# Kernel tuning notes

Hardware: AMD Instinct MI355X
Metric: run time of the kernel (lower is better)

Reference implementation:

```python
import jax, jax.numpy as jnp
import numpy as np

N = 4096      # num_nodes
F = 256       # node_dim
K = 4         # num_heads
FP = 64       # out_dim per head
P_EDGE = 0.008  # edge probability (~33 avg degree)


def setup_inputs() -> dict:
    key = jax.random.key(0)
    k1, k2, k3, k4, k5 = jax.random.split(key, 5)
    x = jax.random.normal(k1, (N, F), dtype=jnp.float32)
    # binary adjacency mask with self loops so every row has a neighbor
    adj = (jax.random.uniform(k2, (N, N)) < P_EDGE).astype(jnp.float32)
    mask = jnp.maximum(adj, jnp.eye(N, dtype=jnp.float32))
    batch = jnp.zeros((N,), dtype=jnp.int32)  # unused (is_final_layer=False)
    # xavier-style init for W (node_dim -> K*FP) and attention vectors
    w_scale = np.sqrt(2.0 / (F + K * FP)).astype(np.float32)
    W = jax.random.normal(k3, (F, K * FP), dtype=jnp.float32) * w_scale
    b = jnp.zeros((K * FP,), dtype=jnp.float32)
    a_scale = np.sqrt(2.0 / (K * FP + 1)).astype(np.float32)
    a_left = jax.random.normal(k4, (1, K, FP), dtype=jnp.float32) * a_scale
    a_right = jax.random.normal(k5, (1, K, FP), dtype=jnp.float32) * a_scale
    return {"x": x, "mask": mask, "batch": batch, "W": W, "b": b,
            "a_left": a_left, "a_right": a_right}


def reference(x, mask, batch, W, b, a_left, a_right):
    # dropout prob = 0.0 (eval mode) -> identity
    x_proj = (x @ W + b).reshape(N, K, FP)                 # (N,K,F')
    score_src = (x_proj * a_left).sum(axis=-1)             # (N,K)
    score_tgt = (x_proj * a_right).sum(axis=-1)            # (N,K)
    score = score_src[:, None, :] + score_tgt[None, :, :]  # (N,N,K)
    score = jax.nn.leaky_relu(score, negative_slope=0.2)
    # non-standard global mean/std normalization (torch .std() is unbiased)
    score = (score - score.mean()) / score.std(ddof=1)
    score = jnp.exp(score)
    m = mask[:, :, None]                                   # (N,N,1)
    denom = (score * m).sum(axis=1, keepdims=True)         # (N,1,K)
    aij = (score / denom) * m                              # (N,N,K)
    attention = jnp.transpose(aij, (2, 0, 1))              # (K,N,N)
    h_prime = jnp.einsum('knm,mkf->nkf', attention, x_proj)  # (N,K,F')
    h_prime = jax.nn.elu(h_prime)
    # is_final_layer=False -> concat heads
    return h_prime.reshape(N, K * FP)
```

## Files before the change

### kernel.cpp

```cpp
#include <hip/hip_runtime.h>
#include <hip/hip_bf16.h>
#include <math.h>

#define NN 4096
#define FF 256
#define KH 4
#define FP 64
#define NCOL 256
#define MAXNBR 512
#define SCAN_BLKS 4096
#define GEMM_BLKS 512
#define MOM_BLOCKS 1024
#define MOM_ROWS 4

__device__ __forceinline__ float bits2f(unsigned b) {
    union { unsigned u; float f; } c; c.u = b << 16; return c.f;
}
__device__ __forceinline__ int is_fp32(const void* mask) {
    return ((const unsigned*)mask)[0] == 0x3F800000u;
}

#define OFF_PART   0
#define OFF_MUSIG  65536
#define OFF_XP     131072
#define OFF_SRC    4325376
#define OFF_TGT    4390912
#define OFF_NBR    4456448
#define OFF_CNT    8650752

__global__ __launch_bounds__(256) void k_scores(
        const void* __restrict__ xr, const void* __restrict__ mask,
        const void* __restrict__ Wr, const void* __restrict__ br,
        const void* __restrict__ alr, const void* __restrict__ arr,
        float* __restrict__ srcb, float* __restrict__ tgtb) {
    const int fl = is_fp32(mask);
    const int tid = threadIdx.x;
    __shared__ float al_s[NCOL], ar_s[NCOL];
    __shared__ float wl_s[FF][KH], wr_s[FF][KH];
    __shared__ float bl_s[KH], brr_s[KH];

    if (fl) {
        al_s[tid] = ((const float*)alr)[tid];
        ar_s[tid] = ((const float*)arr)[tid];
    } else {
        al_s[tid] = bits2f(((const unsigned short*)alr)[tid]);
        ar_s[tid] = bits2f(((const unsigned short*)arr)[tid]);
    }
    __syncthreads();

    if (tid < 8) {
        int k = tid & 3, which = tid >> 2;
        float s = 0.f;
        for (int f = 0; f < FP; ++f) {
            int cc = k * FP + f;
            float bvv = fl ? ((const float*)br)[cc]
                           : bits2f(((const unsigned short*)br)[cc]);
            s += bvv * (which ? ar_s[cc] : al_s[cc]);
        }
        if (which) brr_s[k] = s; else bl_s[k] = s;
    }

    {
        const float* WrowF = (const float*)Wr + (size_t)tid * NCOL;
        const unsigned short* WrowB = (const unsigned short*)Wr + (size_t)tid * NCOL;
        #pragma unroll
        for (int k = 0; k < KH; ++k) {
            float sl = 0.f, sr = 0.f;
            for (int f = 0; f < FP; ++f) {
                int cc = k * FP + f;
                float w = fl ? WrowF[cc] : bits2f(WrowB[cc]);
                sl += w * al_s[cc];
                sr += w * ar_s[cc];
            }
            wl_s[tid][k] = sl;
            wr_s[tid][k] = sr;
        }
    }
    __syncthreads();

    const int r = tid & 63, k = tid >> 6;
    const int n = blockIdx.x * 64 + r;
    float sl = bl_s[k], sr = brr_s[k];
    if (fl) {
        const float4* xrow = (const float4*)((const float*)xr + (size_t)n * FF);
        for (int j4 = 0; j4 < FF / 4; ++j4) {
            float4 xv = xrow[j4];
            int j = j4 * 4;
            sl += xv.x * wl_s[j][k] + xv.y * wl_s[j+1][k] + xv.z * wl_s[j+2][k] + xv.w * wl_s[j+3][k];
            sr += xv.x * wr_s[j][k] + xv.y * wr_s[j+1][k] + xv.z * wr_s[j+2][k] + xv.w * wr_s[j+3][k];
        }
    } else {
        const ushort4* xrow = (const ushort4*)((const unsigned short*)xr + (size_t)n * FF);
        for (int j4 = 0; j4 < FF / 4; ++j4) {
            ushort4 u = xrow[j4];
            float x0 = bits2f(u.x), x1 = bits2f(u.y), x2 = bits2f(u.z), x3 = bits2f(u.w);
            int j = j4 * 4;
            sl += x0 * wl_s[j][k] + x1 * wl_s[j+1][k] + x2 * wl_s[j+2][k] + x3 * wl_s[j+3][k];
            sr += x0 * wr_s[j][k] + x1 * wr_s[j+1][k] + x2 * wr_s[j+2][k] + x3 * wr_s[j+3][k];
        }
    }
    srcb[n * KH + k] = sl;
    tgtb[n * KH + k] = sr;
}

__global__ __launch_bounds__(256) void k_fused(
        const void* __restrict__ xr, const void* __restrict__ mask,
        const void* __restrict__ Wr, const void* __restrict__ br,
        float* __restrict__ xp,
        const float* __restrict__ srcb, const float* __restrict__ tgtb,
        unsigned short* __restrict__ nbr_g, int* __restrict__ cnt_g,
        double2* __restrict__ partials) {
    const int fl = is_fp32(mask);
    const int tid = threadIdx.x;
    __shared__ union {
        float4 xs[8][64];
        struct { unsigned short snbr[MAXNBR]; int cnt; } sc;
        struct { double l1[256], l2[256]; } mo;
    } sm;

    if (blockIdx.x < GEMM_BLKS) {
        int n0 = blockIdx.x * 8;
        if (fl) {
            const float4* xq = (const float4*)xr;
            for (int t = tid; t < 512; t += 256) {
                int r = t >> 6, q = t & 63;
                sm.xs[r][q] = xq[(size_t)(n0 + r) * 64 + q];
            }
        } else {
            const ushort4* xq = (const ushort4*)xr;
            for (int t = tid; t < 512; t += 256) {
                int r = t >> 6, q = t & 63;
                ushort4 u = xq[(size_t)(n0 + r) * 64 + q];
                float4 v; v.x = bits2f(u.x); v.y = bits2f(u.y); v.z = bits2f(u.z); v.w = bits2f(u.w);
                sm.xs[r][q] = v;
            }
        }
        __syncthreads();
        int c = tid;
        float acc[8] = {};
        if (fl) {
            const float* WF = (const float*)Wr;
            for (int kk = 0; kk < 64; ++kk) {
                float w0 = WF[(4 * kk + 0) * NCOL + c];
                float w1 = WF[(4 * kk + 1) * NCOL + c];
                float w2 = WF[(4 * kk + 2) * NCOL + c];
                float w3 = WF[(4 * kk + 3) * NCOL + c];
                #pragma unroll
                for (int r = 0; r < 8; ++r) {
                    float4 xv = sm.xs[r][kk];
                    acc[r] += xv.x * w0 + xv.y * w1 + xv.z * w2 + xv.w * w3;
                }
            }
        } else {
            const unsigned short* WB = (const unsigned short*)Wr;
            for (int kk = 0; kk < 64; ++kk) {
                float w0 = bits2f(WB[(4 * kk + 0) * NCOL + c]);
                float w1 = bits2f(WB[(4 * kk + 1) * NCOL + c]);
                float w2 = bits2f(WB[(4 * kk + 2) * NCOL + c]);
                float w3 = bits2f(WB[(4 * kk + 3) * NCOL + c]);
                #pragma unroll
                for (int r = 0; r < 8; ++r) {
                    float4 xv = sm.xs[r][kk];
                    acc[r] += xv.x * w0 + xv.y * w1 + xv.z * w2 + xv.w * w3;
                }
            }
        }
        float bv = fl ? ((const float*)br)[c] : bits2f(((const unsigned short*)br)[c]);
        #pragma unroll
        for (int r = 0; r < 8; ++r)
            xp[(size_t)(n0 + r) * NCOL + c] = acc[r] + bv;
        return;
    }

    if (blockIdx.x < GEMM_BLKS + MOM_BLOCKS) {
        const int n0 = (blockIdx.x - GEMM_BLKS) * MOM_ROWS;
        const float4* s4 = (const float4*)srcb;
        float4 sv0 = s4[n0 + 0], sv1 = s4[n0 + 1], sv2 = s4[n0 + 2], sv3 = s4[n0 + 3];
        float a1_0 = 0.f, a2_0 = 0.f, a1_1 = 0.f, a2_1 = 0.f;
        float a1_2 = 0.f, a2_2 = 0.f, a1_3 = 0.f, a2_3 = 0.f;
        #pragma unroll 2
        for (int m = tid; m < NN; m += 256) {
            float4 tv = ((const float4*)tgtb)[m];
            #define MROW(sv, A1, A2) { \
                float v0 = sv.x + tv.x; v0 = fmaxf(v0, 0.2f * v0); \
                float v1 = sv.y + tv.y; v1 = fmaxf(v1, 0.2f * v1); \
                float v2 = sv.z + tv.z; v2 = fmaxf(v2, 0.2f * v2); \
                float v3 = sv.w + tv.w; v3 = fmaxf(v3, 0.2f * v3); \
                A1 += (v0 + v1) + (v2 + v3); \
                A2 += (v0 * v0 + v1 * v1) + (v2 * v2 + v3 * v3); }
            MROW(sv0, a1_0, a2_0)
            MROW(sv1, a1_1, a2_1)
            MROW(sv2, a1_2, a2_2)
            MROW(sv3, a1_3, a2_3)
            #undef MROW
        }
        sm.mo.l1[tid] = ((double)a1_0 + (double)a1_1) + ((double)a1_2 + (double)a1_3);
        sm.mo.l2[tid] = ((double)a2_0 + (double)a2_1) + ((double)a2_2 + (double)a2_3);
        __syncthreads();
        for (int off = 128; off; off >>= 1) {
            if (tid < off) {
                sm.mo.l1[tid] += sm.mo.l1[tid + off];
                sm.mo.l2[tid] += sm.mo.l2[tid + off];
            }
            __syncthreads();
        }
        if (tid == 0) {
            double2 pr; pr.x = sm.mo.l1[0]; pr.y = sm.mo.l2[0];
            partials[blockIdx.x - GEMM_BLKS] = pr;
        }
        return;
    }

    int n = blockIdx.x - GEMM_BLKS - MOM_BLOCKS;
    if (tid == 0) sm.sc.cnt = 0;
    __syncthreads();
    if (fl) {
        const uint4* p = (const uint4*)((const float*)mask + (size_t)n * NN);
        for (int i = tid; i < NN / 4; i += 256) {
            uint4 v = p[i]; int base = i * 4;
            if (v.x) { int s = atomicAdd(&sm.sc.cnt, 1); if (s < MAXNBR) sm.sc.snbr[s] = base + 0; }
            if (v.y) { int s = atomicAdd(&sm.sc.cnt, 1); if (s < MAXNBR) sm.sc.snbr[s] = base + 1; }
            if (v.z) { int s = atomicAdd(&sm.sc.cnt, 1); if (s < MAXNBR) sm.sc.snbr[s] = base + 2; }
            if (v.w) { int s = atomicAdd(&sm.sc.cnt, 1); if (s < MAXNBR) sm.sc.snbr[s] = base + 3; }
        }
    } else {
        const uint4* p = (const uint4*)((const unsigned short*)mask + (size_t)n * NN);
        for (int i = tid; i < NN / 8; i += 256) {
            uint4 v = p[i]; int base = i * 8;
            if (v.x & 0xFFFFu) { int s = atomicAdd(&sm.sc.cnt, 1); if (s < MAXNBR) sm.sc.snbr[s] = base + 0; }
            if (v.x >> 16)     { int s = atomicAdd(&sm.sc.cnt, 1); if (s < MAXNBR) sm.sc.snbr[s] = base + 1; }
            if (v.y & 0xFFFFu) { int s = atomicAdd(&sm.sc.cnt, 1); if (s < MAXNBR) sm.sc.snbr[s] = base + 2; }
            if (v.y >> 16)     { int s = atomicAdd(&sm.sc.cnt, 1); if (s < MAXNBR) sm.sc.snbr[s] = base + 3; }
            if (v.z & 0xFFFFu) { int s = atomicAdd(&sm.sc.cnt, 1); if (s < MAXNBR) sm.sc.snbr[s] = base + 4; }
            if (v.z >> 16)     { int s = atomicAdd(&sm.sc.cnt, 1); if (s < MAXNBR) sm.sc.snbr[s] = base + 5; }
            if (v.w & 0xFFFFu) { int s = atomicAdd(&sm.sc.cnt, 1); if (s < MAXNBR) sm.sc.snbr[s] = base + 6; }
            if (v.w >> 16)     { int s = atomicAdd(&sm.sc.cnt, 1); if (s < MAXNBR) sm.sc.snbr[s] = base + 7; }
        }
    }
    __syncthreads();
    int c = sm.sc.cnt < MAXNBR ? sm.sc.cnt : MAXNBR;
    for (int j = tid; j < c; j += 256)
        nbr_g[(size_t)n * MAXNBR + j] = sm.sc.snbr[j];
    if (tid == 0) cnt_g[n] = c;
}

__global__ __launch_bounds__(256) void k_fold(
        const double2* __restrict__ partials, float* __restrict__ musig) {
    double a = 0.0, b2 = 0.0;
    for (int i = threadIdx.x; i < MOM_BLOCKS; i += 256) {
        double2 pr = partials[i];
        a += pr.x; b2 += pr.y;
    }
    __shared__ double l1[256], l2[256];
    l1[threadIdx.x] = a;
    l2[threadIdx.x] = b2;
    __syncthreads();
    for (int off = 128; off; off >>= 1) {
        if (threadIdx.x < off) {
            l1[threadIdx.x] += l1[threadIdx.x + off];
            l2[threadIdx.x] += l2[threadIdx.x + off];
        }
        __syncthreads();
    }
    if (threadIdx.x == 0) {
        double s = l1[0], ss = l2[0];
        const double tot = (double)NN * (double)NN * (double)KH;
        musig[0] = (float)(s / tot);
        musig[1] = (float)(1.0 / sqrt((ss - s * s / tot) / (tot - 1.0)));
    }
}

__global__ __launch_bounds__(256) void k_aggregate(
        const unsigned short* __restrict__ nbr_g, const int* __restrict__ cnt_g,
        const float* __restrict__ musig,
        const float* __restrict__ xp,
        const float* __restrict__ srcb, const float* __restrict__ tgtb,
        float* __restrict__ out) {
    const int tid = threadIdx.x;
    const int wave = tid >> 6, lane = tid & 63;
    __shared__ unsigned short snbr[MAXNBR];
    __shared__ float pls[MAXNBR * KH];
    __shared__ float invden[KH];
    __shared__ float4 red[4][64];
    float mu = musig[0], inv_sigma = musig[1];
    int n = blockIdx.x;
    int c = cnt_g[n];
    for (int j = tid; j < c; j += 256) snbr[j] = nbr_g[(size_t)n * MAXNBR + j];
    __syncthreads();

    for (int t = tid; t < c * KH; t += 256) {
        int j = t >> 2, k = t & 3;
        int m = snbr[j];
        float v = srcb[n * KH + k] + tgtb[m * KH + k];
        v = v > 0.f ? v : 0.2f * v;
        pls[t] = expf((v - mu) * inv_sigma);
    }
    __syncthreads();

    {
        float d = 0.f;
        for (int j = lane; j < c; j += 64) d += pls[j * KH + wave];
        #pragma unroll
        for (int off = 32; off; off >>= 1) d += __shfl_down(d, off, 64);
        if (lane == 0) invden[wave] = 1.0f / d;
    }
    __syncthreads();

    const int k = lane >> 4;
    const float4* xp4 = (const float4*)xp;
    float4 acc = make_float4(0.f, 0.f, 0.f, 0.f);
    int j = wave;
    for (; j + 4 < c; j += 8) {
        int m0 = snbr[j], m1 = snbr[j + 4];
        float w0 = pls[j * KH + k], w1 = pls[(j + 4) * KH + k];
        float4 a = xp4[(size_t)m0 * 64 + lane];
        float4 b = xp4[(size_t)m1 * 64 + lane];
        acc.x += w0 * a.x + w1 * b.x;
        acc.y += w0 * a.y + w1 * b.y;
        acc.z += w0 * a.z + w1 * b.z;
        acc.w += w0 * a.w + w1 * b.w;
    }
    if (j < c) {
        int m0 = snbr[j];
        float w0 = pls[j * KH + k];
        float4 a = xp4[(size_t)m0 * 64 + lane];
        acc.x += w0 * a.x; acc.y += w0 * a.y;
        acc.z += w0 * a.z; acc.w += w0 * a.w;
    }
    red[wave][lane] = acc;
    __syncthreads();
    if (tid < 64) {
        float4 r0 = red[0][tid], r1 = red[1][tid], r2 = red[2][tid], r3 = red[3][tid];
        float s = invden[tid >> 4];
        float4 o;
        o.x = (r0.x + r1.x + r2.x + r3.x) * s;
        o.y = (r0.y + r1.y + r2.y + r3.y) * s;
        o.z = (r0.z + r1.z + r2.z + r3.z) * s;
        o.w = (r0.w + r1.w + r2.w + r3.w) * s;
        o.x = o.x > 0.f ? o.x : expm1f(o.x);
        o.y = o.y > 0.f ? o.y : expm1f(o.y);
        o.z = o.z > 0.f ? o.z : expm1f(o.z);
        o.w = o.w > 0.f ? o.w : expm1f(o.w);
        ((float4*)out)[(size_t)n * 64 + tid] = o;
    }
}

extern "C" void kernel_launch(void* const* d_in, const int* in_sizes, int n_in,
                              void* d_out, int out_size, void* d_ws, size_t ws_size,
                              hipStream_t stream) {
    const void* x    = d_in[0];
    const void* mask = d_in[1];
    const void* W    = d_in[3];
    const void* b    = d_in[4];
    const void* al   = d_in[5];
    const void* ar   = d_in[6];

    char* ws = (char*)d_ws;
    double2* part = (double2*)(ws + OFF_PART);
    float* musig = (float*)(ws + OFF_MUSIG);
    float* xp   = (float*)(ws + OFF_XP);
    float* src  = (float*)(ws + OFF_SRC);
    float* tgt  = (float*)(ws + OFF_TGT);
    unsigned short* nbr = (unsigned short*)(ws + OFF_NBR);
    int* cntg = (int*)(ws + OFF_CNT);

    k_scores<<<64, 256, 0, stream>>>(x, mask, W, b, al, ar, src, tgt);
    k_fused<<<GEMM_BLKS + MOM_BLOCKS + SCAN_BLKS, 256, 0, stream>>>(
        x, mask, W, b, xp, src, tgt, nbr, cntg, part);
    k_fold<<<1, 256, 0, stream>>>(part, musig);
    k_aggregate<<<NN, 256, 0, stream>>>(nbr, cntg, musig, xp, src, tgt,
                                        (float*)d_out);
}
```

Baseline: 184.0 us.

## Split score kernel into W-fold precompute and wave-per-row score kernel

Previously each of 64 blocks redundantly folded W with the attention vectors (256 threads each doing serial 64-length loops over W rows), then one thread per (row, head) walked the whole x row. Now a small 4-block kernel computes the folded W·a vectors once into workspace, and a 512-block scores kernel assigns a wave per row with coalesced x loads and shuffle reductions. This removes the redundant per-block W fold and the uncoalesced strided loads, and raises parallelism, at the cost of one extra kernel launch.

```diff
diff --git a/kernel.cpp b/kernel.cpp
--- a/kernel.cpp
+++ b/kernel.cpp
@@ -27,18 +27,19 @@
 #define OFF_TGT    4390912
 #define OFF_NBR    4456448
 #define OFF_CNT    8650752
-
-__global__ __launch_bounds__(256) void k_scores(
-        const void* __restrict__ xr, const void* __restrict__ mask,
+#define OFF_WLT    8667136
+#define OFF_WRT    8671232
+#define OFF_BB     8675328
+
+__global__ __launch_bounds__(256) void k_prew(
         const void* __restrict__ Wr, const void* __restrict__ br,
         const void* __restrict__ alr, const void* __restrict__ arr,
-        float* __restrict__ srcb, float* __restrict__ tgtb) {
+        const void* __restrict__ mask,
+        float* __restrict__ wlT, float* __restrict__ wrT, float* __restrict__ bb) {
     const int fl = is_fp32(mask);
     const int tid = threadIdx.x;
+    const int wave = tid >> 6, lane = tid & 63;
     __shared__ float al_s[NCOL], ar_s[NCOL];
-    __shared__ float wl_s[FF][KH], wr_s[FF][KH];
-    __shared__ float bl_s[KH], brr_s[KH];
-
     if (fl) {
         al_s[tid] = ((const float*)alr)[tid];
         ar_s[tid] = ((const float*)arr)[tid];
@@ -47,60 +48,94 @@
         ar_s[tid] = bits2f(((const unsigned short*)arr)[tid]);
     }
     __syncthreads();
-
-    if (tid < 8) {
-        int k = tid & 3, which = tid >> 2;
-        float s = 0.f;
-        for (int f = 0; f < FP; ++f) {
-            int cc = k * FP + f;
-            float bvv = fl ? ((const float*)br)[cc]
-                           : bits2f(((const unsigned short*)br)[cc]);
-            s += bvv * (which ? ar_s[cc] : al_s[cc]);
-        }
-        if (which) brr_s[k] = s; else bl_s[k] = s;
-    }
-
-    {
-        const float* WrowF = (const float*)Wr + (size_t)tid * NCOL;
-        const unsigned short* WrowB = (const unsigned short*)Wr + (size_t)tid * NCOL;
+    const float* WF = (const float*)Wr;
+    const unsigned short* WB = (const unsigned short*)Wr;
+    for (int i = 0; i < 16; ++i) {
+        int j = blockIdx.x * 64 + wave * 16 + i;
         #pragma unroll
         for (int k = 0; k < KH; ++k) {
-            float sl = 0.f, sr = 0.f;
-            for (int f = 0; f < FP; ++f) {
-                int cc = k * FP + f;
-                float w = fl ? WrowF[cc] : bits2f(WrowB[cc]);
-                sl += w * al_s[cc];
-                sr += w * ar_s[cc];
-            }
-            wl_s[tid][k] = sl;
-            wr_s[tid][k] = sr;
-        }
-    }
-    __syncthreads();
-
-    const int r = tid & 63, k = tid >> 6;
-    const int n = blockIdx.x * 64 + r;
-    float sl = bl_s[k], sr = brr_s[k];
-    if (fl) {
-        const float4* xrow = (const float4*)((const float*)xr + (size_t)n * FF);
-        for (int j4 = 0; j4 < FF / 4; ++j4) {
-            float4 xv = xrow[j4];
-            int j = j4 * 4;
-            sl += xv.x * wl_s[j][k] + xv.y * wl_s[j+1][k] + xv.z * wl_s[j+2][k] + xv.w * wl_s[j+3][k];
-            sr += xv.x * wr_s[j][k] + xv.y * wr_s[j+1][k] + xv.z * wr_s[j+2][k] + xv.w * wr_s[j+3][k];
-        }
-    } else {
-        const ushort4* xrow = (const ushort4*)((const unsigned short*)xr + (size_t)n * FF);
-        for (int j4 = 0; j4 < FF / 4; ++j4) {
-            ushort4 u = xrow[j4];
-            float x0 = bits2f(u.x), x1 = bits2f(u.y), x2 = bits2f(u.z), x3 = bits2f(u.w);
-            int j = j4 * 4;
-            sl += x0 * wl_s[j][k] + x1 * wl_s[j+1][k] + x2 * wl_s[j+2][k] + x3 * wl_s[j+3][k];
-            sr += x0 * wr_s[j][k] + x1 * wr_s[j+1][k] + x2 * wr_s[j+2][k] + x3 * wr_s[j+3][k];
-        }
-    }
-    srcb[n * KH + k] = sl;
-    tgtb[n * KH + k] = sr;
+            int cc = k * FP + lane;
+            float w = fl ? WF[(size_t)j * NCOL + cc] : bits2f(WB[(size_t)j * NCOL + cc]);
+            float sl = w * al_s[cc];
+            float sr = w * ar_s[cc];
+            #pragma unroll
+            for (int off = 32; off; off >>= 1) {
+                sl += __shfl_down(sl, off, 64);
+                sr += __shfl_down(sr, off, 64);
+            }
+            if (lane == 0) { wlT[k * FF + j] = sl; wrT[k * FF + j] = sr; }
+        }
+    }
+    if (blockIdx.x == 0 && wave == 0) {
+        #pragma unroll
+        for (int k = 0; k < KH; ++k) {
+            int cc = k * FP + lane;
+            float bv = fl ? ((const float*)br)[cc] : bits2f(((const unsigned short*)br)[cc]);
+            float sl = bv * al_s[cc];
+            float sr = bv * ar_s[cc];
+            #pragma unroll
+            for (int off = 32; off; off >>= 1) {
+                sl += __shfl_down(sl, off, 64);
+                sr += __shfl_down(sr, off, 64);
+            }
+            if (lane == 0) { bb[k] = sl; bb[4 + k] = sr; }
+        }
+    }
+}
+
+__global__ __launch_bounds__(256) void k_scores(
+        const void* __restrict__ xr, const void* __restrict__ mask,
+        const float* __restrict__ wlT, const float* __restrict__ wrT,
+        const float* __restrict__ bb,
+        float* __restrict__ srcb, float* __restrict__ tgtb) {
+    const int fl = is_fp32(mask);
+    const int tid = threadIdx.x;
+    const int wave = tid >> 6, lane = tid & 63;
+    __shared__ float wl_s[KH][FF], wr_s[KH][FF];
+    for (int it = 0; it < 4; ++it) {
+        ((float*)wl_s)[it * 256 + tid] = wlT[it * 256 + tid];
+        ((float*)wr_s)[it * 256 + tid] = wrT[it * 256 + tid];
+    }
+    float blv[4], brv[4];
+    #pragma unroll
+    for (int k = 0; k < 4; ++k) { blv[k] = bb[k]; brv[k] = bb[4 + k]; }
+    __syncthreads();
+
+    for (int i = 0; i < 2; ++i) {
+        const int n = blockIdx.x * 8 + wave * 2 + i;
+        float xc0, xc1, xc2, xc3;
+        if (fl) {
+            const float* xrow = (const float*)xr + (size_t)n * FF;
+            xc0 = xrow[lane]; xc1 = xrow[lane + 64];
+            xc2 = xrow[lane + 128]; xc3 = xrow[lane + 192];
+        } else {
+            const unsigned short* xrow = (const unsigned short*)xr + (size_t)n * FF;
+            xc0 = bits2f(xrow[lane]); xc1 = bits2f(xrow[lane + 64]);
+            xc2 = bits2f(xrow[lane + 128]); xc3 = bits2f(xrow[lane + 192]);
+        }
+        float sl[4], sr[4];
+        #pragma unroll
+        for (int k = 0; k < 4; ++k) {
+            sl[k] = xc0 * wl_s[k][lane]       + xc1 * wl_s[k][lane + 64]
+                  + xc2 * wl_s[k][lane + 128] + xc3 * wl_s[k][lane + 192];
+            sr[k] = xc0 * wr_s[k][lane]       + xc1 * wr_s[k][lane + 64]
+                  + xc2 * wr_s[k][lane + 128] + xc3 * wr_s[k][lane + 192];
+        }
+        #pragma unroll
+        for (int off = 32; off; off >>= 1) {
+            #pragma unroll
+            for (int k = 0; k < 4; ++k) {
+                sl[k] += __shfl_down(sl[k], off, 64);
+                sr[k] += __shfl_down(sr[k], off, 64);
+            }
+        }
+        if (lane == 0) {
+            ((float4*)srcb)[n] = make_float4(sl[0] + blv[0], sl[1] + blv[1],
+                                             sl[2] + blv[2], sl[3] + blv[3]);
+            ((float4*)tgtb)[n] = make_float4(sr[0] + brv[0], sr[1] + brv[1],
+                                             sr[2] + brv[2], sr[3] + brv[3]);
+        }
+    }
 }
 
 __global__ __launch_bounds__(256) void k_fused(
@@ -363,8 +398,12 @@
     float* tgt  = (float*)(ws + OFF_TGT);
     unsigned short* nbr = (unsigned short*)(ws + OFF_NBR);
     int* cntg = (int*)(ws + OFF_CNT);
-
-    k_scores<<<64, 256, 0, stream>>>(x, mask, W, b, al, ar, src, tgt);
+    float* wlT = (float*)(ws + OFF_WLT);
+    float* wrT = (float*)(ws + OFF_WRT);
+    float* bb  = (float*)(ws + OFF_BB);
+
+    k_prew<<<4, 256, 0, stream>>>(W, b, al, ar, mask, wlT, wrT, bb);
+    k_scores<<<512, 256, 0, stream>>>(x, mask, wlT, wrT, bb, src, tgt);
     k_fused<<<GEMM_BLKS + MOM_BLOCKS + SCAN_BLKS, 256, 0, stream>>>(
         x, mask, W, b, xp, src, tgt, nbr, cntg, part);
     k_fold<<<1, 256, 0, stream>>>(part, musig);
```

Result: no change. 182.2 us (-1.0%).
